# Kernel optimization log

Measured on AMD Instinct MI355X. Metric: run time of the kernel, lower is better.

## Reference

```python
import jax, jax.numpy as jnp
import numpy as np

INPUT_SIZE = 416.0
CONF_THRESH = 0.25
IOU_THRESH = 0.45
N = 8192


def setup_inputs() -> dict:
    key = jax.random.key(0)
    preds = jax.random.normal(key, (1, 5, N), dtype=jnp.float32)
    return {"preds": preds}


def _pairwise_iou(b):
    # b: [N,4] xyxy -> iou: [N,N], matching the torch clamp(min=0) semantics
    xx1 = jnp.maximum(b[:, None, 0], b[None, :, 0])
    yy1 = jnp.maximum(b[:, None, 1], b[None, :, 1])
    xx2 = jnp.minimum(b[:, None, 2], b[None, :, 2])
    yy2 = jnp.minimum(b[:, None, 3], b[None, :, 3])
    inter = jnp.clip(xx2 - xx1, 0.0) * jnp.clip(yy2 - yy1, 0.0)
    area = jnp.clip(b[:, 2] - b[:, 0], 0.0) * jnp.clip(b[:, 3] - b[:, 1], 0.0)  # [N]
    union = area[:, None] + area[None, :] - inter
    return jnp.where(union > 0, inter / union, 0.0)


def reference(preds):
    # decode: preds [1,5,N] rows = (cx, cy, w, h, obj)
    p = preds[0].T  # [N,5]
    cx, cy, pw, ph, obj = p[:, 0], p[:, 1], p[:, 2], p[:, 3], p[:, 4]
    x1 = cx - pw * 0.5
    y1 = cy - ph * 0.5
    x2 = cx + pw * 0.5
    y2 = cy + ph * 0.5
    boxes = jnp.stack([x1, y1, x2, y2], axis=1)  # [N,4]
    scores = obj
    classes = jnp.zeros_like(scores)

    valid = scores > CONF_THRESH  # conf filter (kept as mask; invalid boxes never kept)
    # scale to absolute coords iff all coords are normalized (max <= 1)
    scale = jnp.where(jnp.max(boxes) <= 1.0, INPUT_SIZE, 1.0)
    boxes_abs = boxes * scale

    # greedy NMS over score-descending order
    order = jnp.argsort(-scores)
    b = boxes_abs[order]          # [N,4]
    s = scores[order]             # [N]
    v = valid[order]              # [N]
    c = classes[order]            # [N]

    iou = _pairwise_iou(b)        # [N,N]

    def step(suppressed, xs):
        iou_row, v_i, i = xs
        keep_i = v_i & jnp.logical_not(suppressed[i])
        suppressed = suppressed | (keep_i & (iou_row > IOU_THRESH))
        return suppressed, keep_i

    _, keep = jax.lax.scan(
        step,
        jnp.zeros((N,), dtype=bool),
        (iou, v, jnp.arange(N)),
    )  # keep: [N] bool, in sorted order

    out = jnp.stack(
        [b[:, 0] / INPUT_SIZE, b[:, 1] / INPUT_SIZE,
         b[:, 2] / INPUT_SIZE, b[:, 3] / INPUT_SIZE, s, c],
        axis=1,
    )  # [N,6]
    # fixed-shape jit-compatible output: suppressed/filtered rows are zeroed;
    # kept rows appear in descending-score order (same order torch compacts to)
    return jnp.where(keep[:, None], out, 0.0)
```

## Files before the change

kernel.cpp:

```cpp
#include <hip/hip_runtime.h>
#include <stdint.h>

typedef unsigned long long u64;
typedef unsigned int u32;

#define NBOX 8192
#define ACMAX 1024
#define NCH 16
#define CONF 0.25f
#define IOU_T 0.45f

#define OFF_BLKMAX 256
#define OFF_RANKP  1024
#define OFF_CX1    (OFF_RANKP + 32 * NBOX * 4)
#define OFF_CY1    (OFF_CX1 + ACMAX * 4)
#define OFF_CX2    (OFF_CX1 + 2 * ACMAX * 4)
#define OFF_CY2    (OFF_CX1 + 3 * ACMAX * 4)
#define OFF_CSC    (OFF_CX1 + 4 * ACMAX * 4)
#define OFF_CAR    (OFF_CX1 + 5 * ACMAX * 4)
#define OFF_ROFC   (OFF_CX1 + 6 * ACMAX * 4)
#define OFF_CMASKT (OFF_CX1 + 7 * ACMAX * 4)

__device__ inline u64 readlane64(u64 v, int l) {
    u32 lo = (u32)__builtin_amdgcn_readlane((int)(u32)v, l);
    u32 hi = (u32)__builtin_amdgcn_readlane((int)(u32)(v >> 32), l);
    return ((u64)hi << 32) | (u64)lo;
}

__global__ void __launch_bounds__(1024) k_rank(
        const float* __restrict__ p, u32* __restrict__ rankp,
        float* __restrict__ blkmax) {
    #pragma clang fp contract(off)
    int t = threadIdx.x;
    int ib = blockIdx.x, jb = blockIdx.y;
    int jbase = jb * 256;
    __shared__ float4 sjv[64];
    __shared__ u64 sact[4];
    __shared__ float redm[4];
    if (t < 64) sjv[t] = ((const float4*)(p + 4 * NBOX + jbase))[t];
    if (t < 256) {
        int j = jbase + t;
        float cx = p[j], cy = p[NBOX + j];
        float pw = p[2 * NBOX + j], ph = p[3 * NBOX + j];
        float obj = p[4 * NBOX + j];
        float hx = pw * 0.5f, hy = ph * 0.5f;
        float x1 = cx - hx, y1 = cy - hy, x2 = cx + hx, y2 = cy + hy;
        bool a = (obj > CONF) && (x2 > x1) && (y2 > y1);
        u64 ab = __ballot(a);
        if ((t & 63) == 0) sact[t >> 6] = ab;
        float m = fmaxf(fmaxf(x1, y1), fmaxf(x2, y2));
        #pragma unroll
        for (int o = 32; o > 0; o >>= 1) m = fmaxf(m, __shfl_xor(m, o, 64));
        if ((t & 63) == 0) redm[t >> 6] = m;
    }
    __syncthreads();
    if (ib == 0 && t == 0)
        blkmax[jb] = fmaxf(fmaxf(redm[0], redm[1]), fmaxf(redm[2], redm[3]));
    int i = ib * 1024 + t;
    float si = p[4 * NBOX + i];
    int cnt = 0, ccnt = 0;
    #pragma unroll
    for (int w = 0; w < 4; w++) {
        u64 aw = sact[w];
        #pragma unroll
        for (int q = 0; q < 16; q++) {
            int tt4 = w * 16 + q;
            float4 v = sjv[tt4];
            int j0 = jbase + tt4 * 4;
            int c0 = ((v.x > si) || (v.x == si && (j0 + 0) < i)) ? 1 : 0;
            int c1 = ((v.y > si) || (v.y == si && (j0 + 1) < i)) ? 1 : 0;
            int c2 = ((v.z > si) || (v.z == si && (j0 + 2) < i)) ? 1 : 0;
            int c3 = ((v.w > si) || (v.w == si && (j0 + 3) < i)) ? 1 : 0;
            cnt += c0 + c1 + c2 + c3;
            int sh = (q << 2);
            ccnt += (c0 & (int)((aw >> (sh + 0)) & 1ull))
                  + (c1 & (int)((aw >> (sh + 1)) & 1ull))
                  + (c2 & (int)((aw >> (sh + 2)) & 1ull))
                  + (c3 & (int)((aw >> (sh + 3)) & 1ull));
        }
    }
    rankp[jb * NBOX + i] = (u32)cnt | ((u32)ccnt << 16);
}

__global__ void __launch_bounds__(1024) k_scatter(
        const float* __restrict__ p, const u32* __restrict__ rankp,
        const float* __restrict__ blkmax,
        float* __restrict__ cx1, float* __restrict__ cy1,
        float* __restrict__ cx2, float* __restrict__ cy2,
        float* __restrict__ csc, float* __restrict__ car,
        int* __restrict__ rofc, float* __restrict__ out) {
    #pragma clang fp contract(off)
    int i = blockIdx.x * 1024 + threadIdx.x;
    u32 acc = 0;
    #pragma unroll
    for (int jb = 0; jb < 32; jb++) acc += rankp[jb * NBOX + i];
    int r = (int)(acc & 0xFFFFu);
    int cr = (int)(acc >> 16);
    float m = blkmax[0];
    #pragma unroll
    for (int k = 1; k < 32; k++) m = fmaxf(m, blkmax[k]);
    float scale = (m <= 1.0f) ? 416.0f : 1.0f;
    float cx = p[i], cy = p[NBOX + i];
    float pw = p[2 * NBOX + i], ph = p[3 * NBOX + i];
    float s = p[4 * NBOX + i];
    float hx = pw * 0.5f, hy = ph * 0.5f;
    float x1 = cx - hx, y1 = cy - hy, x2 = cx + hx, y2 = cy + hy;
    bool a = (s > CONF) && (x2 > x1) && (y2 > y1);
    float bx1 = x1 * scale, by1 = y1 * scale;
    float bx2 = x2 * scale, by2 = y2 * scale;
    float aw = fmaxf(bx2 - bx1, 0.0f);
    float ah = fmaxf(by2 - by1, 0.0f);
    float area = aw * ah;
    bool ok = a && (cr < ACMAX);
    if (ok) {
        cx1[cr] = bx1; cy1[cr] = by1; cx2[cr] = bx2; cy2[cr] = by2;
        csc[cr] = s; car[cr] = area; rofc[cr] = r;
    } else {
        bool valid = s > CONF;
        float* o = out + (size_t)r * 6;
        o[0] = valid ? bx1 / 416.0f : 0.0f;
        o[1] = valid ? by1 / 416.0f : 0.0f;
        o[2] = valid ? bx2 / 416.0f : 0.0f;
        o[3] = valid ? by2 / 416.0f : 0.0f;
        o[4] = valid ? s : 0.0f;
        o[5] = 0.0f;
    }
}

__global__ void __launch_bounds__(64) k_mask(
        const float* __restrict__ cx1, const float* __restrict__ cy1,
        const float* __restrict__ cx2, const float* __restrict__ cy2,
        const float* __restrict__ car, const float* __restrict__ csc,
        u64* __restrict__ cmaskT) {
    #pragma clang fp contract(off)
    int t = threadIdx.x;
    int i0 = blockIdx.x * 64, j0 = blockIdx.y * 64;
    u64 rv = __ballot(csc[i0 + t] > CONF);
    u64 cv = __ballot(csc[j0 + t] > CONF);
    if (rv == 0ull || cv == 0ull) return;
    __shared__ float sx1[64], sy1[64], sx2[64], sy2[64], sa[64];
    sx1[t] = cx1[i0 + t]; sy1[t] = cy1[i0 + t];
    sx2[t] = cx2[i0 + t]; sy2[t] = cy2[i0 + t];
    sa[t] = car[i0 + t];
    __syncthreads();
    int j = j0 + t;
    float xj1 = cx1[j], yj1 = cy1[j], xj2 = cx2[j], yj2 = cy2[j], aj = car[j];
    u64 w = 0;
    for (int ii = 0; ii < 64; ii++) {
        float xx1 = fmaxf(sx1[ii], xj1);
        float yy1 = fmaxf(sy1[ii], yj1);
        float xx2 = fminf(sx2[ii], xj2);
        float yy2 = fminf(sy2[ii], yj2);
        float iw = fmaxf(xx2 - xx1, 0.0f);
        float ih = fmaxf(yy2 - yy1, 0.0f);
        float inter = iw * ih;
        float uni = sa[ii] + aj - inter;
        bool sup = (uni > 0.0f) && (inter / uni > IOU_T);
        w |= ((u64)(sup ? 1u : 0u)) << ii;
    }
    cmaskT[(size_t)blockIdx.x * ACMAX + j] = w;
}

__global__ void __launch_bounds__(1024) k_final(
        const float* __restrict__ csc, const u64* __restrict__ cmaskT,
        const float* __restrict__ cx1, const float* __restrict__ cy1,
        const float* __restrict__ cx2, const float* __restrict__ cy2,
        const int* __restrict__ rofc, float* __restrict__ out) {
    int t = threadIdx.x;
    __shared__ u64 keptArr[NCH];
    int wv = t >> 6;
    float s = csc[t];
    bool valid = s > CONF;
    u64 col[NCH];
    #pragma unroll
    for (int w = 0; w < NCH; w++) col[w] = cmaskT[(size_t)w * ACMAX + t];
    bool sup = false;
    for (int c = 0; c < NCH; c++) {
        if (wv == c) {
            u64 validm = __ballot(valid);
            u64 supm = __ballot(sup);
            u64 d = col[c];
            u64 kept = 0;
            u64 cand = validm & ~supm;
            while (cand) {
                int i = __builtin_ctzll(cand);
                kept |= (1ull << i);
                u64 row = readlane64(d, i);
                u64 gt = (i < 63) ? (~0ull << (i + 1)) : 0ull;
                cand = cand & ~row & gt;
            }
            if ((t & 63) == 0) keptArr[c] = kept;
        }
        __syncthreads();
        u64 k = keptArr[c];
        if (wv > c && (col[c] & k) != 0ull) sup = true;
    }
    __syncthreads();
    if (valid) {
        bool kb = (keptArr[t >> 6] >> (t & 63)) & 1ull;
        int r = rofc[t];
        float* o = out + (size_t)r * 6;
        o[0] = kb ? cx1[t] / 416.0f : 0.0f;
        o[1] = kb ? cy1[t] / 416.0f : 0.0f;
        o[2] = kb ? cx2[t] / 416.0f : 0.0f;
        o[3] = kb ? cy2[t] / 416.0f : 0.0f;
        o[4] = kb ? s : 0.0f;
        o[5] = 0.0f;
    }
}

extern "C" void kernel_launch(void* const* d_in, const int* in_sizes, int n_in,
                              void* d_out, int out_size, void* d_ws, size_t ws_size,
                              hipStream_t stream) {
    const float* preds = (const float*)d_in[0];
    float* out = (float*)d_out;
    char* ws = (char*)d_ws;
    float* blkmax = (float*)(ws + OFF_BLKMAX);
    u32* rankp    = (u32*)(ws + OFF_RANKP);
    float* cx1 = (float*)(ws + OFF_CX1);
    float* cy1 = (float*)(ws + OFF_CY1);
    float* cx2 = (float*)(ws + OFF_CX2);
    float* cy2 = (float*)(ws + OFF_CY2);
    float* csc = (float*)(ws + OFF_CSC);
    float* car = (float*)(ws + OFF_CAR);
    int* rofc  = (int*)(ws + OFF_ROFC);
    u64* cmaskT = (u64*)(ws + OFF_CMASKT);

    hipLaunchKernelGGL(k_rank, dim3(8, 32), dim3(1024), 0, stream,
                       preds, rankp, blkmax);
    hipLaunchKernelGGL(k_scatter, dim3(8), dim3(1024), 0, stream,
                       preds, rankp, blkmax,
                       cx1, cy1, cx2, cy2, csc, car, rofc, out);
    hipLaunchKernelGGL(k_mask, dim3(NCH, NCH), dim3(64), 0, stream,
                       cx1, cy1, cx2, cy2, car, csc, cmaskT);
    hipLaunchKernelGGL(k_final, dim3(1), dim3(1024), 0, stream,
                       csc, cmaskT, cx1, cy1, cx2, cy2, rofc, out);
}
```

Baseline: 111.4 us.

## Fuse rank and scatter kernels into one packed-key rank-counting sort kernel

Replaces the two-kernel rank computation, which wrote 32 partial rank arrays to global memory and then summed them, with a single kernel of 256 blocks. Each block ranks 32 boxes against all 8192 by comparing packed 64-bit keys (order-preserving encoded score plus reversed index), and adds the active-box count through a multiplier packed in the low bits. Each block also recomputes the global coordinate max itself and does the scatter directly. This removes one launch and the global partial-rank round trip, but every block now reloads all inputs and repeats the max reduction.

```diff
diff --git a/kernel.cpp b/kernel.cpp
--- a/kernel.cpp
+++ b/kernel.cpp
@@ -10,9 +10,7 @@
 #define CONF 0.25f
 #define IOU_T 0.45f
 
-#define OFF_BLKMAX 256
-#define OFF_RANKP  1024
-#define OFF_CX1    (OFF_RANKP + 32 * NBOX * 4)
+#define OFF_CX1    256
 #define OFF_CY1    (OFF_CX1 + ACMAX * 4)
 #define OFF_CX2    (OFF_CX1 + 2 * ACMAX * 4)
 #define OFF_CY2    (OFF_CX1 + 3 * ACMAX * 4)
@@ -27,103 +25,121 @@
     return ((u64)hi << 32) | (u64)lo;
 }
 
-__global__ void __launch_bounds__(1024) k_rank(
-        const float* __restrict__ p, u32* __restrict__ rankp,
-        float* __restrict__ blkmax) {
-    #pragma clang fp contract(off)
-    int t = threadIdx.x;
-    int ib = blockIdx.x, jb = blockIdx.y;
-    int jbase = jb * 256;
-    __shared__ float4 sjv[64];
-    __shared__ u64 sact[4];
-    __shared__ float redm[4];
-    if (t < 64) sjv[t] = ((const float4*)(p + 4 * NBOX + jbase))[t];
-    if (t < 256) {
-        int j = jbase + t;
-        float cx = p[j], cy = p[NBOX + j];
-        float pw = p[2 * NBOX + j], ph = p[3 * NBOX + j];
-        float obj = p[4 * NBOX + j];
-        float hx = pw * 0.5f, hy = ph * 0.5f;
-        float x1 = cx - hx, y1 = cy - hy, x2 = cx + hx, y2 = cy + hy;
-        bool a = (obj > CONF) && (x2 > x1) && (y2 > y1);
-        u64 ab = __ballot(a);
-        if ((t & 63) == 0) sact[t >> 6] = ab;
-        float m = fmaxf(fmaxf(x1, y1), fmaxf(x2, y2));
-        #pragma unroll
-        for (int o = 32; o > 0; o >>= 1) m = fmaxf(m, __shfl_xor(m, o, 64));
-        if ((t & 63) == 0) redm[t >> 6] = m;
-    }
-    __syncthreads();
-    if (ib == 0 && t == 0)
-        blkmax[jb] = fmaxf(fmaxf(redm[0], redm[1]), fmaxf(redm[2], redm[3]));
-    int i = ib * 1024 + t;
-    float si = p[4 * NBOX + i];
-    int cnt = 0, ccnt = 0;
-    #pragma unroll
-    for (int w = 0; w < 4; w++) {
-        u64 aw = sact[w];
-        #pragma unroll
-        for (int q = 0; q < 16; q++) {
-            int tt4 = w * 16 + q;
-            float4 v = sjv[tt4];
-            int j0 = jbase + tt4 * 4;
-            int c0 = ((v.x > si) || (v.x == si && (j0 + 0) < i)) ? 1 : 0;
-            int c1 = ((v.y > si) || (v.y == si && (j0 + 1) < i)) ? 1 : 0;
-            int c2 = ((v.z > si) || (v.z == si && (j0 + 2) < i)) ? 1 : 0;
-            int c3 = ((v.w > si) || (v.w == si && (j0 + 3) < i)) ? 1 : 0;
-            cnt += c0 + c1 + c2 + c3;
-            int sh = (q << 2);
-            ccnt += (c0 & (int)((aw >> (sh + 0)) & 1ull))
-                  + (c1 & (int)((aw >> (sh + 1)) & 1ull))
-                  + (c2 & (int)((aw >> (sh + 2)) & 1ull))
-                  + (c3 & (int)((aw >> (sh + 3)) & 1ull));
-        }
-    }
-    rankp[jb * NBOX + i] = (u32)cnt | ((u32)ccnt << 16);
-}
-
-__global__ void __launch_bounds__(1024) k_scatter(
-        const float* __restrict__ p, const u32* __restrict__ rankp,
-        const float* __restrict__ blkmax,
+__device__ inline u32 encf(float f) {
+    u32 u = __float_as_uint(f);
+    return (u & 0x80000000u) ? ~u : (u | 0x80000000u);
+}
+
+__global__ void __launch_bounds__(1024) k_sort(
+        const float* __restrict__ p,
         float* __restrict__ cx1, float* __restrict__ cy1,
         float* __restrict__ cx2, float* __restrict__ cy2,
         float* __restrict__ csc, float* __restrict__ car,
         int* __restrict__ rofc, float* __restrict__ out) {
     #pragma clang fp contract(off)
-    int i = blockIdx.x * 1024 + threadIdx.x;
-    u32 acc = 0;
-    #pragma unroll
-    for (int jb = 0; jb < 32; jb++) acc += rankp[jb * NBOX + i];
-    int r = (int)(acc & 0xFFFFu);
-    int cr = (int)(acc >> 16);
-    float m = blkmax[0];
-    #pragma unroll
-    for (int k = 1; k < 32; k++) m = fmaxf(m, blkmax[k]);
-    float scale = (m <= 1.0f) ? 416.0f : 1.0f;
-    float cx = p[i], cy = p[NBOX + i];
-    float pw = p[2 * NBOX + i], ph = p[3 * NBOX + i];
-    float s = p[4 * NBOX + i];
-    float hx = pw * 0.5f, hy = ph * 0.5f;
-    float x1 = cx - hx, y1 = cy - hy, x2 = cx + hx, y2 = cy + hy;
-    bool a = (s > CONF) && (x2 > x1) && (y2 > y1);
-    float bx1 = x1 * scale, by1 = y1 * scale;
-    float bx2 = x2 * scale, by2 = y2 * scale;
-    float aw = fmaxf(bx2 - bx1, 0.0f);
-    float ah = fmaxf(by2 - by1, 0.0f);
-    float area = aw * ah;
-    bool ok = a && (cr < ACMAX);
-    if (ok) {
-        cx1[cr] = bx1; cy1[cr] = by1; cx2[cr] = bx2; cy2[cr] = by2;
-        csc[cr] = s; car[cr] = area; rofc[cr] = r;
-    } else {
-        bool valid = s > CONF;
-        float* o = out + (size_t)r * 6;
-        o[0] = valid ? bx1 / 416.0f : 0.0f;
-        o[1] = valid ? by1 / 416.0f : 0.0f;
-        o[2] = valid ? bx2 / 416.0f : 0.0f;
-        o[3] = valid ? by2 / 416.0f : 0.0f;
-        o[4] = valid ? s : 0.0f;
-        o[5] = 0.0f;
+    int t = threadIdx.x;
+    int b = blockIdx.x;
+    __shared__ u64 keys[1024];
+    __shared__ u32 accs[128][36];
+    __shared__ u32 accs2[8][32];
+    __shared__ float redm[16];
+    __shared__ float s_gmax;
+
+    int il4 = (t & 7) * 4;
+    int js  = t >> 3;
+    int ibase = b * 32;
+
+    u64 Ki[4];
+    #pragma unroll
+    for (int q = 0; q < 4; q++) {
+        int i = ibase + il4 + q;
+        u32 e = encf(p[4 * NBOX + i]);
+        Ki[q] = ((u64)e << 32) | ((u64)(8191 - i) << 19) | 0x1FFFFull;
+    }
+
+    u32 acc[4] = {0u, 0u, 0u, 0u};
+    float mloc = -3.4e38f;
+    for (int w = 0; w < 8; w++) {
+        int j = w * 1024 + t;
+        float cxj = p[j], cyj = p[NBOX + j];
+        float pwj = p[2 * NBOX + j], phj = p[3 * NBOX + j];
+        float sj = p[4 * NBOX + j];
+        float hx = pwj * 0.5f, hy = phj * 0.5f;
+        float x1 = cxj - hx, y1 = cyj - hy, x2 = cxj + hx, y2 = cyj + hy;
+        bool act = (sj > CONF) && (x2 > x1) && (y2 > y1);
+        mloc = fmaxf(mloc, fmaxf(fmaxf(x1, y1), fmaxf(x2, y2)));
+        u32 e = encf(sj);
+        u32 mult = act ? 65537u : 1u;
+        __syncthreads();
+        keys[t] = ((u64)e << 32) | ((u64)(8191 - j) << 19) | (u64)mult;
+        __syncthreads();
+        int base = js * 8;
+        #pragma unroll
+        for (int k2 = 0; k2 < 4; k2++) {
+            u64 ka = keys[base + k2 * 2];
+            u64 kb = keys[base + k2 * 2 + 1];
+            u32 ma = (u32)ka & 0x1FFFFu;
+            u32 mb = (u32)kb & 0x1FFFFu;
+            #pragma unroll
+            for (int q = 0; q < 4; q++) {
+                acc[q] += (ka > Ki[q]) ? ma : 0u;
+                acc[q] += (kb > Ki[q]) ? mb : 0u;
+            }
+        }
+    }
+    #pragma unroll
+    for (int q = 0; q < 4; q++) accs[js][il4 + q] = acc[q];
+    #pragma unroll
+    for (int o = 32; o > 0; o >>= 1) mloc = fmaxf(mloc, __shfl_xor(mloc, o, 64));
+    if ((t & 63) == 0) redm[t >> 6] = mloc;
+    __syncthreads();
+    if (t < 256) {
+        int il = t & 31, part = t >> 5;
+        u32 s = 0;
+        #pragma unroll
+        for (int q = 0; q < 16; q++) s += accs[part * 16 + q][il];
+        accs2[part][il] = s;
+    }
+    if (t == 0) {
+        float g = redm[0];
+        #pragma unroll
+        for (int k = 1; k < 16; k++) g = fmaxf(g, redm[k]);
+        s_gmax = g;
+    }
+    __syncthreads();
+    if (t < 32) {
+        u32 total = 0;
+        #pragma unroll
+        for (int part = 0; part < 8; part++) total += accs2[part][t];
+        int r = (int)(total & 0xFFFFu);
+        int cr = (int)(total >> 16);
+        int i = ibase + t;
+        float scale = (s_gmax <= 1.0f) ? 416.0f : 1.0f;
+        float cx = p[i], cy = p[NBOX + i];
+        float pw = p[2 * NBOX + i], ph = p[3 * NBOX + i];
+        float s = p[4 * NBOX + i];
+        float hx = pw * 0.5f, hy = ph * 0.5f;
+        float x1 = cx - hx, y1 = cy - hy, x2 = cx + hx, y2 = cy + hy;
+        bool a = (s > CONF) && (x2 > x1) && (y2 > y1);
+        float bx1 = x1 * scale, by1 = y1 * scale;
+        float bx2 = x2 * scale, by2 = y2 * scale;
+        float aw = fmaxf(bx2 - bx1, 0.0f);
+        float ah = fmaxf(by2 - by1, 0.0f);
+        float area = aw * ah;
+        bool ok = a && (cr < ACMAX);
+        if (ok) {
+            cx1[cr] = bx1; cy1[cr] = by1; cx2[cr] = bx2; cy2[cr] = by2;
+            csc[cr] = s; car[cr] = area; rofc[cr] = r;
+        } else {
+            bool valid = s > CONF;
+            float* o = out + (size_t)r * 6;
+            o[0] = valid ? bx1 / 416.0f : 0.0f;
+            o[1] = valid ? by1 / 416.0f : 0.0f;
+            o[2] = valid ? bx2 / 416.0f : 0.0f;
+            o[3] = valid ? by2 / 416.0f : 0.0f;
+            o[4] = valid ? s : 0.0f;
+            o[5] = 0.0f;
+        }
     }
 }
 
@@ -215,8 +231,6 @@
     const float* preds = (const float*)d_in[0];
     float* out = (float*)d_out;
     char* ws = (char*)d_ws;
-    float* blkmax = (float*)(ws + OFF_BLKMAX);
-    u32* rankp    = (u32*)(ws + OFF_RANKP);
     float* cx1 = (float*)(ws + OFF_CX1);
     float* cy1 = (float*)(ws + OFF_CY1);
     float* cx2 = (float*)(ws + OFF_CX2);
@@ -226,11 +240,8 @@
     int* rofc  = (int*)(ws + OFF_ROFC);
     u64* cmaskT = (u64*)(ws + OFF_CMASKT);
 
-    hipLaunchKernelGGL(k_rank, dim3(8, 32), dim3(1024), 0, stream,
-                       preds, rankp, blkmax);
-    hipLaunchKernelGGL(k_scatter, dim3(8), dim3(1024), 0, stream,
-                       preds, rankp, blkmax,
-                       cx1, cy1, cx2, cy2, csc, car, rofc, out);
+    hipLaunchKernelGGL(k_sort, dim3(256), dim3(1024), 0, stream,
+                       preds, cx1, cy1, cx2, cy2, csc, car, rofc, out);
     hipLaunchKernelGGL(k_mask, dim3(NCH, NCH), dim3(64), 0, stream,
                        cx1, cy1, cx2, cy2, car, csc, cmaskT);
     hipLaunchKernelGGL(k_final, dim3(1), dim3(1024), 0, stream,
```

Result: faster. 102.2 us (-8.2%).
